# Kernel tuning notes

Measured on AMD Instinct MI355X. Metric: run time of the kernel, lower is better.

The kernel has to match this reference:

```python
import jax, jax.numpy as jnp
import numpy as np

B, N, K, H, NF = 4, 4096, 20, 64, 128
EPS = 1e-5  # BatchNorm eps (inference mode)


def _knn_idx(x):
    # x: (B, C, N); returns indices of K nearest neighbors (incl. self), (B, N, K)
    xx = jnp.sum(x * x, axis=1)                      # (B, N)
    inner = jnp.einsum('bcn,bcm->bnm', x, x)         # (B, N, N)
    neg_dist = 2.0 * inner - xx[:, :, None] - xx[:, None, :]
    return jax.lax.top_k(neg_dist, K)[1]


def _graph_feat(x, first):
    # x: (B, C, N) -> edge features (B, C', N, K)
    idx = _knn_idx(x)                                # (B, N, K)
    xt = jnp.transpose(x, (0, 2, 1))                 # (B, N, C)
    nb = jax.vmap(lambda f, i: f[i])(xt, idx)        # (B, N, K, C)
    nb = jnp.transpose(nb, (0, 3, 1, 2))             # (B, C, N, K)
    c = jnp.broadcast_to(x[:, :, :, None], nb.shape)
    parts = [nb - c]
    if first:  # cross term only in first block (3-dim coords)
        parts.append(jnp.cross(c, nb, axis=1))
    parts.append(c)
    return jnp.concatenate(parts, axis=1)


def _conv_bn_lrelu(x, W, g, b, m, v):
    # 1x1 conv (no bias) + BatchNorm (inference) + LeakyReLU(0.2)
    y = jnp.einsum('oc,bc...->bo...', W, x)
    scale = g / jnp.sqrt(v + EPS)
    sh = (1, -1) + (1,) * (y.ndim - 2)
    y = y * scale.reshape(sh) + (b - m * scale).reshape(sh)
    return jnp.where(y >= 0, y, 0.2 * y)


def _forward(x, layers, We, Wh, bh):
    x = jnp.transpose(x, (0, 2, 1))                  # (B, 3, N)
    outs = []
    for li in range(4):
        gf = _graph_feat(x, li == 0)                 # (B, cin, N, K)
        y = _conv_bn_lrelu(gf, *layers[li])          # (B, cout, N, K)
        x = jnp.max(y, axis=-1)                      # max-pool over neighbors
        outs.append(x)
    cat = jnp.concatenate(outs, axis=1)              # (B, 512, N)
    y = _conv_bn_lrelu(cat, *layers[4])              # final Conv1d block
    y = jnp.max(y, axis=-1)                          # global max over points
    emb = y @ We.T                                   # Linear(512, NF, bias=False)
    return emb @ Wh.T + bh                           # embedding_head


def setup_inputs() -> dict:
    key = jax.random.key(0)
    ks = jax.random.split(key, 40)

    def nrm(k, shape, s=0.1):
        return jax.random.normal(k, shape, jnp.float32) * s

    inp = {'x': jax.random.normal(ks[0], (B, N, 3), jnp.float32)}
    dims = [(9, H), (2 * H, H), (2 * H, 2 * H), (4 * H, 4 * H), (8 * H, 8 * H)]
    i = 1
    for li, (cin, cout) in enumerate(dims):
        inp['W%d' % li] = nrm(ks[i], (cout, cin)); i += 1
        inp['g%d' % li] = 1.0 + nrm(ks[i], (cout,), 0.05); i += 1
        inp['b%d' % li] = nrm(ks[i], (cout,), 0.05); i += 1
        inp['m%d' % li] = nrm(ks[i], (cout,), 0.05); i += 1
        inp['v%d' % li] = 1.0 + jax.random.uniform(ks[i], (cout,)) * 0.1; i += 1
    inp['We'] = nrm(ks[i], (NF, 8 * H)); i += 1
    inp['Wh'] = nrm(ks[i], (NF, NF)); i += 1
    inp['bh'] = nrm(ks[i], (NF,))
    return inp


def reference(x, W0, g0, b0, m0, v0, W1, g1, b1, m1, v1, W2, g2, b2, m2, v2,
              W3, g3, b3, m3, v3, W4, g4, b4, m4, v4, We, Wh, bh):
    layers = [(W0, g0, b0, m0, v0), (W1, g1, b1, m1, v1), (W2, g2, b2, m2, v2),
              (W3, g3, b3, m3, v3), (W4, g4, b4, m4, v4)]
    return _forward(x, layers, We, Wh, bh)
```

## Files before the change

### kernel.cpp

```cpp
#include <hip/hip_runtime.h>
#include <cfloat>

#define N_PTS 4096
#define NB    4
#define KNN   20
#define EPSB  1e-5f
#define NSL   4

typedef short s8v __attribute__((ext_vector_type(8)));
typedef float f4v __attribute__((ext_vector_type(4)));

__device__ __forceinline__ void bf16split(float x, unsigned short* h, unsigned short* l)
{
    unsigned u = __builtin_bit_cast(unsigned, x);
    unsigned hb = (u + 0x7fffu + ((u >> 16) & 1u)) >> 16;
    float hf = __builtin_bit_cast(float, hb << 16);
    float res = x - hf;
    unsigned u2 = __builtin_bit_cast(unsigned, res);
    unsigned lb = (u2 + 0x7fffu + ((u2 >> 16) & 1u)) >> 16;
    *h = (unsigned short)hb;
    *l = (unsigned short)lb;
}

__device__ __forceinline__ unsigned packkey(float d, int lc)
{
    d = fmaxf(d, 0.f);
    unsigned u = __builtin_bit_cast(unsigned, d);
    return (u & 0xFFFFFF00u) | (unsigned)lc;
}

__device__ __forceinline__ void insert20k(unsigned key, unsigned (&k20)[KNN])
{
#pragma unroll
    for (int j = 0; j < KNN; j++) {
        unsigned old = k20[j];
        unsigned lo = old < key ? old : key;
        key = old < key ? key : old;
        k20[j] = lo;
    }
}

__device__ __forceinline__ void gl2lds16(const void* g, void* l)
{
    __builtin_amdgcn_global_load_lds(
        (const __attribute__((address_space(1))) unsigned int*)g,
        (__attribute__((address_space(3))) unsigned int*)l,
        16, 0, 0);
}

__device__ __forceinline__ int swz(int g)
{
    return g ^ (((g >> 3) ^ (g >> 6)) & 7);
}

__global__ __launch_bounds__(256)
void to_bf16_pm(const float* __restrict__ F, long bsF, int ldF, int C, int KDP,
                unsigned short* __restrict__ Ghi, unsigned short* __restrict__ Glo)
{
    int b = blockIdx.y;
    int n = blockIdx.x * 64 + (threadIdx.x & 63);
    int kq = threadIdx.x >> 6;
    const float* Fr = F + (long)b * bsF + (long)n * ldF;
    for (int k0 = kq * 8; k0 < KDP; k0 += 32) {
        s8v hv, lv;
#pragma unroll
        for (int i = 0; i < 8; i++) {
            int k = k0 + i;
            float x = (k < C) ? Fr[k] : 0.f;
            unsigned short h, l;
            bf16split(x, &h, &l);
            hv[i] = (short)h;
            lv[i] = (short)l;
        }
        long o = ((long)b * N_PTS + n) * KDP + k0;
        *(s8v*)&Ghi[o] = hv;
        *(s8v*)&Glo[o] = lv;
    }
}

__global__ void sqnorm_pm(const float* __restrict__ F, float* __restrict__ xx,
                          int C, int ldF, long bsF)
{
    int b = blockIdx.y;
    int i = blockIdx.x * 256 + threadIdx.x;
    const float* r = F + (long)b * bsF + (long)i * ldF;
    float s = 0.f;
    for (int c = 0; c < C; c++) s = fmaf(r[c], r[c], s);
    xx[(long)b * N_PTS + i] = s;
}

template<int KDP>
__global__ __launch_bounds__(256, 3)
void fused_knn_mfma7(const unsigned short* __restrict__ Ghi,
                     const unsigned short* __restrict__ Glo,
                     const float* __restrict__ xx,
                     float* __restrict__ knnd, int* __restrict__ knni)
{
    constexpr int KS = KDP / 32;
    constexpr int TS = 16 * KDP;
    constexpr int NCH = (TS * 2) / 16;
    __shared__ short cbuf[2][2][TS];
    __shared__ unsigned mk[4][16][4][KNN];

    int tid = threadIdx.x;
    int w = tid >> 6, L = tid & 63;
    int n = L & 15;
    int quad = L >> 4;
    int b = blockIdx.z, slice = blockIdx.y;
    int q0 = blockIdx.x * 64, qw = w * 16;
    const unsigned short* Gh = Ghi + (long)b * N_PTS * KDP;
    const unsigned short* Gl = Glo + (long)b * N_PTS * KDP;
    const float* xxb = xx + (long)b * N_PTS;

    s8v qhi[KS], qlo[KS];
    long qbase = (long)(q0 + qw + n) * KDP + quad * 8;
#pragma unroll
    for (int ks = 0; ks < KS; ks++) {
        qhi[ks] = *(const s8v*)&Gh[qbase + ks * 32];
        qlo[ks] = *(const s8v*)&Gl[qbase + ks * 32];
    }
    float xq = xxb[q0 + qw + n];

    unsigned k20[KNN];
#pragma unroll
    for (int j = 0; j < KNN; j++) k20[j] = 0xFFFFFFFFu;

    int po[KS];
#pragma unroll
    for (int ks = 0; ks < KS; ks++) {
        int gL = n * (KDP / 8) + quad + ks * 4;
        po[ks] = swz(gL) * 8;
    }
    int gsrc = swz(tid);

    int w64 = tid & 192;
    {
        long tb = (long)(slice * 1024) * KDP;
        if (tid < NCH) {
            gl2lds16((const char*)(Gh + tb) + gsrc * 16,
                     (char*)&cbuf[0][0][0] + w64 * 16);
            gl2lds16((const char*)(Gl + tb) + gsrc * 16,
                     (char*)&cbuf[0][1][0] + w64 * 16);
        }
    }
    __syncthreads();

    const float* xcp = xxb + slice * 1024 + quad * 4;

    for (int t = 0; t < 64; t++) {
        int cur = t & 1;
        if (t < 63 && tid < NCH) {
            long tb = (long)(slice * 1024 + (t + 1) * 16) * KDP;
            gl2lds16((const char*)(Gh + tb) + gsrc * 16,
                     (char*)&cbuf[cur ^ 1][0][0] + w64 * 16);
            gl2lds16((const char*)(Gl + tb) + gsrc * 16,
                     (char*)&cbuf[cur ^ 1][1][0] + w64 * 16);
        }

        const short* Ch = &cbuf[cur][0][0];
        const short* Cl = &cbuf[cur][1][0];
        f4v acc = {0.f, 0.f, 0.f, 0.f};
#pragma unroll
        for (int ks = 0; ks < KS; ks++) {
            s8v chi = *(const s8v*)&Ch[po[ks]];
            s8v clo = *(const s8v*)&Cl[po[ks]];
            acc = __builtin_amdgcn_mfma_f32_16x16x32_bf16(chi, qhi[ks], acc, 0, 0, 0);
            acc = __builtin_amdgcn_mfma_f32_16x16x32_bf16(chi, qlo[ks], acc, 0, 0, 0);
            acc = __builtin_amdgcn_mfma_f32_16x16x32_bf16(clo, qhi[ks], acc, 0, 0, 0);
        }
        float4 xc4 = *(const float4*)xcp;
        float xcv[4] = {xc4.x, xc4.y, xc4.z, xc4.w};
#pragma unroll
        for (int r = 0; r < 4; r++) {
            float d = xq + xcv[r] - 2.f * acc[r];
            insert20k(packkey(d, t * 4 + r), k20);
        }
        xcp += 16;
        __syncthreads();
    }

#pragma unroll
    for (int j = 0; j < KNN; j++) mk[w][n][quad][j] = k20[j];
    __syncthreads();
    if (L < 16) {
        int p[4] = {0, 0, 0, 0};
        long o = (((long)b * NSL + slice) * N_PTS + (q0 + qw + L)) * KNN;
#pragma unroll
        for (int j = 0; j < KNN; j++) {
            unsigned bd = 0xFFFFFF00u; int bi = 0x7fffffff; int bq = 0;
#pragma unroll
            for (int qd = 0; qd < 4; qd++) {
                unsigned kk = mk[w][L][qd][p[qd]];
                unsigned db = kk & 0xFFFFFF00u;
                int lc = (int)(kk & 0xFFu);
                int ci = slice * 1024 + (lc >> 2) * 16 + qd * 4 + (lc & 3);
                if (db < bd || (db == bd && ci < bi)) { bd = db; bi = ci; bq = qd; }
            }
            knnd[o + j] = __builtin_bit_cast(float, bd);
            knni[o + j] = bi;
            p[bq]++;
        }
    }
}

__global__ void knn_merge4(const float* __restrict__ knnd, const int* __restrict__ knni,
                           int* __restrict__ idxOut)
{
    int id = blockIdx.x * 256 + threadIdx.x;
    int b = id / N_PTS, i = id % N_PTS;
    const float* dl[NSL]; const int* il[NSL];
#pragma unroll
    for (int qt = 0; qt < NSL; qt++) {
        dl[qt] = knnd + (((long)b * NSL + qt) * N_PTS + i) * KNN;
        il[qt] = knni + (((long)b * NSL + qt) * N_PTS + i) * KNN;
    }
    int p[NSL];
#pragma unroll
    for (int qt = 0; qt < NSL; qt++) p[qt] = 0;
    int* o = idxOut + (long)id * KNN;
#pragma unroll
    for (int j = 0; j < KNN; j++) {
        float best = FLT_MAX; int bi = 0x7fffffff; int bq = 0;
#pragma unroll
        for (int qt = 0; qt < NSL; qt++) {
            float vv = (p[qt] < KNN) ? dl[qt][p[qt]] : FLT_MAX;
            int   ci = (p[qt] < KNN) ? il[qt][p[qt]] : 0x7fffffff;
            if (vv < best || (vv == best && ci < bi)) { best = vv; bi = ci; bq = qt; }
        }
        o[j] = bi;
        p[bq]++;
    }
}

template<int KDP>
__global__ __launch_bounds__(256)
void qp_mfma(const unsigned short* __restrict__ Ghi,
             const unsigned short* __restrict__ Glo,
             const unsigned short* __restrict__ Wqh, const unsigned short* __restrict__ Wql,
             const unsigned short* __restrict__ Wph, const unsigned short* __restrict__ Wpl,
             const float* __restrict__ shf,
             float* __restrict__ qv, float* __restrict__ pv, int cout)
{
    constexpr int KS = KDP / 32;
    int tid = threadIdx.x;
    int w = tid >> 6, L = tid & 63;
    int n = L & 15, quad = L >> 4;
    int b = blockIdx.z;
    int p0 = blockIdx.x * 64 + w * 16;

    s8v ah[KS], al[KS];
    long abase = ((long)b * N_PTS + p0 + n) * KDP + quad * 8;
#pragma unroll
    for (int ks = 0; ks < KS; ks++) {
        ah[ks] = *(const s8v*)&Ghi[abase + ks * 32];
        al[ks] = *(const s8v*)&Glo[abase + ks * 32];
    }

#pragma unroll
    for (int oc4 = 0; oc4 < 4; oc4++) {
        int oc = blockIdx.y * 4 + oc4;
        long wbase = (long)(oc * 16 + n) * KDP + quad * 8;
        f4v aq = {0.f, 0.f, 0.f, 0.f};
        f4v ap = {0.f, 0.f, 0.f, 0.f};
#pragma unroll
        for (int ks = 0; ks < KS; ks++) {
            s8v wh = *(const s8v*)&Wqh[wbase + ks * 32];
            s8v wl = *(const s8v*)&Wql[wbase + ks * 32];
            aq = __builtin_amdgcn_mfma_f32_16x16x32_bf16(ah[ks], wh, aq, 0, 0, 0);
            aq = __builtin_amdgcn_mfma_f32_16x16x32_bf16(ah[ks], wl, aq, 0, 0, 0);
            aq = __builtin_amdgcn_mfma_f32_16x16x32_bf16(al[ks], wh, aq, 0, 0, 0);
            s8v ph = *(const s8v*)&Wph[wbase + ks * 32];
            s8v pl = *(const s8v*)&Wpl[wbase + ks * 32];
            ap = __builtin_amdgcn_mfma_f32_16x16x32_bf16(ah[ks], ph, ap, 0, 0, 0);
            ap = __builtin_amdgcn_mfma_f32_16x16x32_bf16(ah[ks], pl, ap, 0, 0, 0);
            ap = __builtin_amdgcn_mfma_f32_16x16x32_bf16(al[ks], ph, ap, 0, 0, 0);
        }
        float sv = shf[oc * 16 + n];
#pragma unroll
        for (int r = 0; r < 4; r++) {
            long pt = p0 + quad * 4 + r;
            long o = ((long)b * N_PTS + pt) * cout + oc * 16 + n;
            qv[o] = aq[r];
            pv[o] = ap[r] + sv;
        }
    }
}

__global__ __launch_bounds__(256)
void conv4f_mfma(const float* __restrict__ cat,
                 const unsigned short* __restrict__ W4h, const unsigned short* __restrict__ W4l,
                 const float* __restrict__ shf, float* __restrict__ Y)
{
    int tid = threadIdx.x;
    int w = tid >> 6, L = tid & 63;
    int n = L & 15, quad = L >> 4;
    int b = blockIdx.y;
    int p0 = blockIdx.x * 16;
    const float* cr = cat + ((long)b * N_PTS + p0 + n) * 512 + quad * 8;

    f4v acc[8];
#pragma unroll
    for (int ch = 0; ch < 8; ch++) acc[ch] = {0.f, 0.f, 0.f, 0.f};

    for (int ks = 0; ks < 16; ks++) {
        float4 f0 = *(const float4*)&cr[ks * 32];
        float4 f1 = *(const float4*)&cr[ks * 32 + 4];
        float fv[8] = {f0.x, f0.y, f0.z, f0.w, f1.x, f1.y, f1.z, f1.w};
        s8v bh, bl;
#pragma unroll
        for (int i = 0; i < 8; i++) {
            unsigned short h, l;
            bf16split(fv[i], &h, &l);
            bh[i] = (short)h;
            bl[i] = (short)l;
        }
#pragma unroll
        for (int ch = 0; ch < 8; ch++) {
            long o = (long)((w * 8 + ch) * 16 + n) * 512 + quad * 8 + ks * 32;
            s8v ahv = *(const s8v*)&W4h[o];
            s8v alv = *(const s8v*)&W4l[o];
            acc[ch] = __builtin_amdgcn_mfma_f32_16x16x32_bf16(ahv, bh, acc[ch], 0, 0, 0);
            acc[ch] = __builtin_amdgcn_mfma_f32_16x16x32_bf16(ahv, bl, acc[ch], 0, 0, 0);
            acc[ch] = __builtin_amdgcn_mfma_f32_16x16x32_bf16(alv, bh, acc[ch], 0, 0, 0);
        }
    }
#pragma unroll
    for (int ch = 0; ch < 8; ch++) {
#pragma unroll
        for (int r = 0; r < 4; r++) {
            int o = (w * 8 + ch) * 16 + quad * 4 + r;
            float y = acc[ch][r] + shf[o];
            y = y >= 0.f ? y : 0.2f * y;
            Y[((long)b * 512 + o) * N_PTS + p0 + n] = y;
        }
    }
}

__global__ void fold_edge_bf16(const float* __restrict__ W, const float* __restrict__ g,
                               const float* __restrict__ bb, const float* __restrict__ m,
                               const float* __restrict__ v,
                               unsigned short* __restrict__ Wqh, unsigned short* __restrict__ Wql,
                               unsigned short* __restrict__ Wph, unsigned short* __restrict__ Wpl,
                               float* __restrict__ shift, int C, int cout)
{
    int id = blockIdx.x * 256 + threadIdx.x;
    if (id < C * cout) {
        int o = id / C;
        int c = id % C;
        float sc = g[o] * rsqrtf(v[o] + EPSB);
        float wd = W[(long)o * 2 * C + c];
        float wc = W[(long)o * 2 * C + C + c];
        bf16split(sc * wd, &Wqh[id], &Wql[id]);
        bf16split(sc * (wc - wd), &Wph[id], &Wpl[id]);
    }
    if (id < cout) {
        float sc = g[id] * rsqrtf(v[id] + EPSB);
        shift[id] = bb[id] - m[id] * sc;
    }
}

__global__ void fold_plain_bf16(const float* __restrict__ W, const float* __restrict__ g,
                                const float* __restrict__ bb, const float* __restrict__ m,
                                const float* __restrict__ v,
                                unsigned short* __restrict__ W4h, unsigned short* __restrict__ W4l,
                                float* __restrict__ shift, int C, int cout)
{
    int id = blockIdx.x * 256 + threadIdx.x;
    if (id < C * cout) {
        int o = id / C;
        int c = id % C;
        float sc = g[o] * rsqrtf(v[o] + EPSB);
        bf16split(sc * W[(long)o * C + c], &W4h[id], &W4l[id]);
    }
    if (id < cout) {
        float sc = g[id] * rsqrtf(v[id] + EPSB);
        shift[id] = bb[id] - m[id] * sc;
    }
}

__global__ void gather_max_fused(const float* __restrict__ q, const float* __restrict__ p,
                                 const int* __restrict__ idx, float* __restrict__ cat,
                                 int cout, int c_off,
                                 unsigned short* __restrict__ Ghi,
                                 unsigned short* __restrict__ Glo,
                                 float* __restrict__ xx)
{
    int b = blockIdx.y;
    int i = blockIdx.x * 4 + threadIdx.y;
    int tx = threadIdx.x;
    const int* ip = idx + ((long)b * N_PTS + i) * KNN;
    int js[KNN];
#pragma unroll
    for (int k = 0; k < KNN; k++) js[k] = ip[k];
    const float* qb = q + (long)b * N_PTS * cout;
    const float* pb = p + ((long)b * N_PTS + i) * cout;
    float* ob = cat + ((long)b * N_PTS + i) * 512 + c_off;
    float ssum = 0.f;
    for (int o0 = 0; o0 < cout; o0 += 64) {
        int o = o0 + tx;
        float pv = pb[o];
        float mx = -FLT_MAX;
#pragma unroll
        for (int k = 0; k < KNN; k++) {
            float val = qb[(long)js[k] * cout + o] + pv;
            val = val >= 0.f ? val : 0.2f * val;
            mx = fmaxf(mx, val);
        }
        ob[o] = mx;
        if (Ghi) {
            unsigned short h, l;
            bf16split(mx, &h, &l);
            long go = ((long)b * N_PTS + i) * cout + o;
            Ghi[go] = h;
            Glo[go] = l;
            ssum = fmaf(mx, mx, ssum);
        }
    }
    if (Ghi) {
#pragma unroll
        for (int off = 32; off > 0; off >>= 1) ssum += __shfl_xor(ssum, off);
        if (tx == 0) xx[(long)b * N_PTS + i] = ssum;
    }
}

__global__ void edge0_fused(const float* __restrict__ x, const int* __restrict__ idx,
                            const float* __restrict__ W0, const float* __restrict__ g0,
                            const float* __restrict__ b0, const float* __restrict__ m0,
                            const float* __restrict__ v0, float* __restrict__ cat,
                            unsigned short* __restrict__ Ghi,
                            unsigned short* __restrict__ Glo,
                            float* __restrict__ xx)
{
    int b = blockIdx.y;
    int i = blockIdx.x * 4 + threadIdx.y;
    int o = threadIdx.x;
    const float* xc = x + ((long)b * N_PTS + i) * 3;
    float cx = xc[0], cy = xc[1], cz = xc[2];
    float w[9];
#pragma unroll
    for (int c = 0; c < 9; c++) w[c] = W0[o * 9 + c];
    float sc = g0[o] * rsqrtf(v0[o] + EPSB);
    float sh = b0[o] - m0[o] * sc;
    const int* ip = idx + ((long)b * N_PTS + i) * KNN;
    float mx = -FLT_MAX;
#pragma unroll
    for (int k = 0; k < KNN; k++) {
        const float* xn = x + ((long)b * N_PTS + ip[k]) * 3;
        float nx = xn[0], ny = xn[1], nz = xn[2];
        float dx = nx - cx, dy = ny - cy, dz = nz - cz;
        float crx = cy * nz - cz * ny;
        float cry = cz * nx - cx * nz;
        float crz = cx * ny - cy * nx;
        float y = w[0] * dx + w[1] * dy + w[2] * dz
                + w[3] * crx + w[4] * cry + w[5] * crz
                + w[6] * cx + w[7] * cy + w[8] * cz;
        y = y * sc + sh;
        y = y >= 0.f ? y : 0.2f * y;
        mx = fmaxf(mx, y);
    }
    cat[((long)b * N_PTS + i) * 512 + o] = mx;
    unsigned short h, l;
    bf16split(mx, &h, &l);
    long go = ((long)b * N_PTS + i) * 64 + o;
    Ghi[go] = h;
    Glo[go] = l;
    float ssum = mx * mx;
#pragma unroll
    for (int off = 32; off > 0; off >>= 1) ssum += __shfl_xor(ssum, off);
    if (o == 0) xx[(long)b * N_PTS + i] = ssum;
}

__global__ void rowmax_kernel(const float* __restrict__ Y, float* __restrict__ ymax)
{
    __shared__ float red[256];
    int b = blockIdx.y, o = blockIdx.x, t = threadIdx.x;
    const float* yb = Y + ((long)b * 512 + o) * N_PTS;
    float mx = -FLT_MAX;
#pragma unroll
    for (int s = 0; s < N_PTS / 256; s++) mx = fmaxf(mx, yb[t + 256 * s]);
    red[t] = mx;
    __syncthreads();
    for (int off = 128; off > 0; off >>= 1) {
        if (t < off) red[t] = fmaxf(red[t], red[t + off]);
        __syncthreads();
    }
    if (t == 0) ymax[(long)b * 512 + o] = red[0];
}

__global__ void head_kernel(const float* __restrict__ ymax, const float* __restrict__ We,
                            const float* __restrict__ Wh, const float* __restrict__ bh,
                            float* __restrict__ out)
{
    __shared__ float emb[128];
    __shared__ float yv[512];
    int b = blockIdx.x, t = threadIdx.x;
    for (int s = t; s < 512; s += 128) yv[s] = ymax[(long)b * 512 + s];
    __syncthreads();
    float acc = 0.f;
    for (int c = 0; c < 512; c++) acc = fmaf(yv[c], We[(long)t * 512 + c], acc);
    emb[t] = acc;
    __syncthreads();
    float acc2 = bh[t];
    for (int ff = 0; ff < 128; ff++) acc2 = fmaf(emb[ff], Wh[(long)t * 128 + ff], acc2);
    out[(long)b * 128 + t] = acc2;
}

extern "C" void kernel_launch(void* const* d_in, const int* in_sizes, int n_in,
                              void* d_out, int out_size, void* d_ws, size_t ws_size,
                              hipStream_t stream)
{
    const float* x = (const float*)d_in[0];
    const float *W[5], *g[5], *bb[5], *m[5], *v[5];
    for (int li = 0; li < 5; li++) {
        W[li]  = (const float*)d_in[1 + li * 5 + 0];
        g[li]  = (const float*)d_in[1 + li * 5 + 1];
        bb[li] = (const float*)d_in[1 + li * 5 + 2];
        m[li]  = (const float*)d_in[1 + li * 5 + 3];
        v[li]  = (const float*)d_in[1 + li * 5 + 4];
    }
    const float* We = (const float*)d_in[26];
    const float* Wh = (const float*)d_in[27];
    const float* bh = (const float*)d_in[28];
    float* out = (float*)d_out;

    float* ws   = (float*)d_ws;
    float* cat  = ws;
    float* qbuf = cat + (long)8388608;
    float* pbuf = qbuf + (long)8388608;
    int*   idxb = (int*)(pbuf + 4194304);
    float* xx   = (float*)(idxb + 327680);
    unsigned short* Wqh = (unsigned short*)(xx + 16384);
    unsigned short* Wql = Wqh + 32768;
    unsigned short* Wph = Wql + 32768;
    unsigned short* Wpl = Wph + 32768;
    unsigned short* W4h = Wpl + 32768;
    unsigned short* W4l = W4h + 262144;
    float* shf  = (float*)(W4l + 262144);
    float* ymax = shf + 512;
    unsigned short* Ghi = (unsigned short*)qbuf;
    unsigned short* Glo = Ghi + 2097152;
    float* knnd = qbuf + 2097152;
    int*   knni = (int*)(qbuf + 2097152 + 1310720);
    float* qv   = qbuf + 2097152;
    float* Ybuf = qbuf;

    sqnorm_pm<<<dim3(16, NB), dim3(256), 0, stream>>>(x, xx, 3, 3, (long)3 * N_PTS);
    to_bf16_pm<<<dim3(64, NB), dim3(256), 0, stream>>>(
        x, (long)3 * N_PTS, 3, 3, 32, Ghi, Glo);
    fused_knn_mfma7<32><<<dim3(64, NSL, NB), dim3(256), 0, stream>>>(
        Ghi, Glo, xx, knnd, knni);
    knn_merge4<<<dim3(64), dim3(256), 0, stream>>>(knnd, knni, idxb);
    edge0_fused<<<dim3(N_PTS / 4, NB), dim3(64, 4), 0, stream>>>(
        x, idxb, W[0], g[0], bb[0], m[0], v[0], cat, Ghi, Glo, xx);

    const int Cs_[3]   = {64, 64, 128};
    const int co_[3]   = {64, 128, 256};
    const int outO_[3] = {64, 128, 256};
    for (int s = 0; s < 3; s++) {
        int C = Cs_[s], cout = co_[s];
        if (C == 64)
            fused_knn_mfma7<64><<<dim3(64, NSL, NB), dim3(256), 0, stream>>>(
                Ghi, Glo, xx, knnd, knni);
        else
            fused_knn_mfma7<128><<<dim3(64, NSL, NB), dim3(256), 0, stream>>>(
                Ghi, Glo, xx, knnd, knni);
        knn_merge4<<<dim3(64), dim3(256), 0, stream>>>(knnd, knni, idxb);

        int li = s + 1;
        fold_edge_bf16<<<dim3((C * cout + 255) / 256), dim3(256), 0, stream>>>(
            W[li], g[li], bb[li], m[li], v[li], Wqh, Wql, Wph, Wpl, shf, C, cout);
        if (C == 64)
            qp_mfma<64><<<dim3(64, cout / 64, NB), dim3(256), 0, stream>>>(
                Ghi, Glo, Wqh, Wql, Wph, Wpl, shf, qv, pbuf, cout);
        else
            qp_mfma<128><<<dim3(64, cout / 64, NB), dim3(256), 0, stream>>>(
                Ghi, Glo, Wqh, Wql, Wph, Wpl, shf, qv, pbuf, cout);
        if (s < 2)
            gather_max_fused<<<dim3(N_PTS / 4, NB), dim3(64, 4), 0, stream>>>(
                qv, pbuf, idxb, cat, cout, outO_[s], Ghi, Glo, xx);
        else
            gather_max_fused<<<dim3(N_PTS / 4, NB), dim3(64, 4), 0, stream>>>(
                qv, pbuf, idxb, cat, cout, outO_[s],
                (unsigned short*)nullptr, (unsigned short*)nullptr, (float*)nullptr);
    }

    fold_plain_bf16<<<dim3((512 * 512 + 255) / 256), dim3(256), 0, stream>>>(
        W[4], g[4], bb[4], m[4], v[4], W4h, W4l, shf, 512, 512);
    conv4f_mfma<<<dim3(N_PTS / 16, NB), dim3(256), 0, stream>>>(
        cat, W4h, W4l, shf, Ybuf);

    rowmax_kernel<<<dim3(512, NB), dim3(256), 0, stream>>>(Ybuf, ymax);
    head_kernel<<<dim3(NB), dim3(128), 0, stream>>>(ymax, We, Wh, bh, out);
}
```

Measured before the change: 1.062 ms.

## Retile final conv so each block covers 64 points by 64 output channels

The final 512x512 pointwise conv is retiled. Before, each block took 16 points and every wave covered 128 output channels. Now the grid is points/64 x 8 channel groups x batch, and each wave handles 16 points by 64 channels, with the MFMA operand roles swapped so activations form the A operand. This changes which data each wave reuses and gives each lane fewer accumulators and more blocks to schedule. The cost is that activations are reloaded and re-split into bf16 once for each of the 8 channel groups, and the transposed writes to Y are now strided.

```diff
diff --git a/kernel.cpp b/kernel.cpp
--- a/kernel.cpp
+++ b/kernel.cpp
@@ -287,51 +287,55 @@
 }
 
 __global__ __launch_bounds__(256)
-void conv4f_mfma(const float* __restrict__ cat,
+void conv4g_mfma(const float* __restrict__ cat,
                  const unsigned short* __restrict__ W4h, const unsigned short* __restrict__ W4l,
                  const float* __restrict__ shf, float* __restrict__ Y)
 {
     int tid = threadIdx.x;
     int w = tid >> 6, L = tid & 63;
     int n = L & 15, quad = L >> 4;
-    int b = blockIdx.y;
-    int p0 = blockIdx.x * 16;
+    int b = blockIdx.z;
+    int p0 = blockIdx.x * 64 + w * 16;
+    int ob0 = blockIdx.y * 64;
+
     const float* cr = cat + ((long)b * N_PTS + p0 + n) * 512 + quad * 8;
 
-    f4v acc[8];
-#pragma unroll
-    for (int ch = 0; ch < 8; ch++) acc[ch] = {0.f, 0.f, 0.f, 0.f};
+    f4v acc[4];
+#pragma unroll
+    for (int c4 = 0; c4 < 4; c4++) acc[c4] = {0.f, 0.f, 0.f, 0.f};
 
     for (int ks = 0; ks < 16; ks++) {
         float4 f0 = *(const float4*)&cr[ks * 32];
         float4 f1 = *(const float4*)&cr[ks * 32 + 4];
         float fv[8] = {f0.x, f0.y, f0.z, f0.w, f1.x, f1.y, f1.z, f1.w};
-        s8v bh, bl;
+        s8v ah, al;
 #pragma unroll
         for (int i = 0; i < 8; i++) {
             unsigned short h, l;
             bf16split(fv[i], &h, &l);
-            bh[i] = (short)h;
-            bl[i] = (short)l;
-        }
-#pragma unroll
-        for (int ch = 0; ch < 8; ch++) {
-            long o = (long)((w * 8 + ch) * 16 + n) * 512 + quad * 8 + ks * 32;
-            s8v ahv = *(const s8v*)&W4h[o];
-            s8v alv = *(const s8v*)&W4l[o];
-            acc[ch] = __builtin_amdgcn_mfma_f32_16x16x32_bf16(ahv, bh, acc[ch], 0, 0, 0);
-            acc[ch] = __builtin_amdgcn_mfma_f32_16x16x32_bf16(ahv, bl, acc[ch], 0, 0, 0);
-            acc[ch] = __builtin_amdgcn_mfma_f32_16x16x32_bf16(alv, bh, acc[ch], 0, 0, 0);
-        }
-    }
-#pragma unroll
-    for (int ch = 0; ch < 8; ch++) {
+            ah[i] = (short)h;
+            al[i] = (short)l;
+        }
+#pragma unroll
+        for (int c4 = 0; c4 < 4; c4++) {
+            long wb = (long)(ob0 + c4 * 16 + n) * 512 + quad * 8 + ks * 32;
+            s8v wh = *(const s8v*)&W4h[wb];
+            s8v wl = *(const s8v*)&W4l[wb];
+            acc[c4] = __builtin_amdgcn_mfma_f32_16x16x32_bf16(ah, wh, acc[c4], 0, 0, 0);
+            acc[c4] = __builtin_amdgcn_mfma_f32_16x16x32_bf16(ah, wl, acc[c4], 0, 0, 0);
+            acc[c4] = __builtin_amdgcn_mfma_f32_16x16x32_bf16(al, wh, acc[c4], 0, 0, 0);
+        }
+    }
+#pragma unroll
+    for (int c4 = 0; c4 < 4; c4++) {
+        int o = ob0 + c4 * 16 + n;
+        float sv = shf[o];
 #pragma unroll
         for (int r = 0; r < 4; r++) {
-            int o = (w * 8 + ch) * 16 + quad * 4 + r;
-            float y = acc[ch][r] + shf[o];
+            int pt = p0 + quad * 4 + r;
+            float y = acc[c4][r] + sv;
             y = y >= 0.f ? y : 0.2f * y;
-            Y[((long)b * 512 + o) * N_PTS + p0 + n] = y;
+            Y[((long)b * 512 + o) * N_PTS + pt] = y;
         }
     }
 }
@@ -586,7 +590,7 @@
 
     fold_plain_bf16<<<dim3((512 * 512 + 255) / 256), dim3(256), 0, stream>>>(
         W[4], g[4], bb[4], m[4], v[4], W4h, W4l, shf, 512, 512);
-    conv4f_mfma<<<dim3(N_PTS / 16, NB), dim3(256), 0, stream>>>(
+    conv4g_mfma<<<dim3(N_PTS / 64, 8, NB), dim3(256), 0, stream>>>(
         cat, W4h, W4l, shf, Ybuf);
 
     rowmax_kernel<<<dim3(512, NB), dim3(256), 0, stream>>>(Ybuf, ymax);
```

New measurement: 1.084 ms. 1.02x slower.
